# Optimization experiments

Measured on AMD Instinct MI355X. Metric: run time of the kernel, lower is better.

Reference implementation:

```python
import jax, jax.numpy as jnp
import numpy as np

HID = 128; H = 8; D = HID // H; L = 2; IN = 128; OUT = 32
ND = 20000; NF = 50000; E = 400000
SQRT_D = float(np.sqrt(D))
LN_EPS = 1e-5


def setup_inputs() -> dict:
    key = jax.random.key(0)
    ks = jax.random.split(key, 16)
    s = 1.0 / np.sqrt(HID)
    n = lambda k, sh, sc=1.0: jax.random.normal(k, sh, jnp.float32) * sc
    return dict(
        x_device=n(ks[0], (ND, IN)),
        x_feature=n(ks[1], (NF, IN)),
        e_df_src=jax.random.randint(ks[2], (E,), 0, ND),
        e_df_dst=jax.random.randint(ks[3], (E,), 0, NF),
        e_fd_src=jax.random.randint(ks[4], (E,), 0, NF),
        e_fd_dst=jax.random.randint(ks[5], (E,), 0, ND),
        W_dev_in=n(ks[6], (IN, HID), s), b_dev_in=jnp.zeros((HID,), jnp.float32),
        W_feat_in=n(ks[7], (IN, HID), s), b_feat_in=jnp.zeros((HID,), jnp.float32),
        Wk=n(ks[8], (L, 2, HID, HID), s), bk=jnp.zeros((L, 2, HID), jnp.float32),
        Wq=n(ks[9], (L, 2, HID, HID), s), bq=jnp.zeros((L, 2, HID), jnp.float32),
        Wv=n(ks[10], (L, 2, HID, HID), s), bv=jnp.zeros((L, 2, HID), jnp.float32),
        a_rel=n(ks[11], (L, 2, H, D, D), 1.0 / np.sqrt(D)),
        m_rel=n(ks[12], (L, 2, H, D, D), 1.0 / np.sqrt(D)),
        p_rel=jnp.ones((L, 2, H), jnp.float32),
        Wa=n(ks[13], (L, 2, HID, HID), s), ba=jnp.zeros((L, 2, HID), jnp.float32),
        skip=jnp.ones((L, 2), jnp.float32),
        ln_g=jnp.ones((L, 2, HID), jnp.float32), ln_b=jnp.zeros((L, 2, HID), jnp.float32),
        W_out=n(ks[14], (HID, OUT), s), b_out=jnp.zeros((OUT,), jnp.float32),
    )


def _layer_norm(x, g, b):
    m = x.mean(-1, keepdims=True)
    v = ((x - m) ** 2).mean(-1, keepdims=True)
    return (x - m) * jax.lax.rsqrt(v + LN_EPS) * g + b


def _edge_agg(q_dst, k_src, v_src, a_r, m_r, p_r, src, dst, n_dst):
    # per-edge-type relation transforms of source k/v: [N_src,H,D]
    kt = jnp.einsum('nhd,hde->nhe', k_src, a_r)
    vt = jnp.einsum('nhd,hde->nhe', v_src, m_r)
    # per-edge attention logits [E,H], scaled by relation prior
    logit = (q_dst[dst] * kt[src]).sum(-1) * p_r / SQRT_D
    # segment softmax over incoming edges of each dst node (per edge type)
    mx = jax.ops.segment_max(logit, dst, num_segments=n_dst)
    ex = jnp.exp(logit - mx[dst])
    sm = jax.ops.segment_sum(ex, dst, num_segments=n_dst)
    alpha = ex / (sm[dst] + 1e-16)
    # attention-weighted message scatter-sum -> [n_dst,H,D]
    return jax.ops.segment_sum(vt[src] * alpha[..., None], dst, num_segments=n_dst)


def _forward(x_device, x_feature, W_dev_in, b_dev_in, W_feat_in, b_feat_in,
             Wk, bk, Wq, bq, Wv, bv, a_rel, m_rel, p_rel, Wa, ba, skip,
             ln_g, ln_b, W_out, b_out, e_df_src, e_df_dst, e_fd_src, e_fd_dst):
    x_d = jax.nn.relu(x_device @ W_dev_in + b_dev_in)
    x_f = jax.nn.relu(x_feature @ W_feat_in + b_feat_in)
    for l in range(L):
        xs = (x_d, x_f)  # node-type 0 = device, 1 = feature
        k = [(xs[t] @ Wk[l, t] + bk[l, t]).reshape(-1, H, D) for t in range(2)]
        q = [(xs[t] @ Wq[l, t] + bq[l, t]).reshape(-1, H, D) for t in range(2)]
        v = [(xs[t] @ Wv[l, t] + bv[l, t]).reshape(-1, H, D) for t in range(2)]
        # edge type 0: device -> feature ; edge type 1: feature -> device
        agg_f = _edge_agg(q[1], k[0], v[0], a_rel[l, 0], m_rel[l, 0], p_rel[l, 0],
                          e_df_src, e_df_dst, NF)
        agg_d = _edge_agg(q[0], k[1], v[1], a_rel[l, 1], m_rel[l, 1], p_rel[l, 1],
                          e_fd_src, e_fd_dst, ND)
        new = []
        for t, agg in ((0, agg_d), (1, agg_f)):
            o = jax.nn.gelu(agg.reshape(-1, HID), approximate=False) @ Wa[l, t] + ba[l, t]
            sk = jax.nn.sigmoid(skip[l, t])
            o = sk * o + (1.0 - sk) * xs[t]              # HGTConv skip
            new.append(_layer_norm(xs[t] + o, ln_g[l, t], ln_b[l, t]))  # wrapper residual+LN (dropout=identity in eval)
        x_d, x_f = new
    return x_d @ W_out + b_out


def reference(x_device, x_feature, e_df_src, e_df_dst, e_fd_src, e_fd_dst,
              W_dev_in, b_dev_in, W_feat_in, b_feat_in, Wk, bk, Wq, bq, Wv, bv,
              a_rel, m_rel, p_rel, Wa, ba, skip, ln_g, ln_b, W_out, b_out):
    return _forward(x_device, x_feature, W_dev_in, b_dev_in, W_feat_in, b_feat_in,
                    Wk, bk, Wq, bq, Wv, bv, a_rel, m_rel, p_rel, Wa, ba, skip,
                    ln_g, ln_b, W_out, b_out, e_df_src, e_df_dst, e_fd_src, e_fd_dst)
```

## Files before the change

### kernel.cpp

```cpp
#include <hip/hip_runtime.h>
#include <math.h>

#define ND 20000
#define NF 50000
#define NE 400000
#define NT (NF + ND)
#define NBKT 256
#define BKTW 274

typedef __attribute__((ext_vector_type(8))) short short8;
typedef __attribute__((ext_vector_type(4))) float f32x4;
typedef unsigned short us;

static __device__ __forceinline__ us f2bf(float f) {
    unsigned u = __builtin_bit_cast(unsigned, f);
    u += 0x7FFF + ((u >> 16) & 1);
    return (us)(u >> 16);
}
static __device__ __forceinline__ float bf2f(us h) {
    return __builtin_bit_cast(float, (unsigned)h << 16);
}
static __device__ __forceinline__ float bflo(unsigned u) {
    return __builtin_bit_cast(float, u << 16);
}
static __device__ __forceinline__ float bfhi(unsigned u) {
    return __builtin_bit_cast(float, u & 0xFFFF0000u);
}
static __device__ __forceinline__ float gelu_f(float x) {
    return 0.5f * x * (1.0f + erff(x * 0.70710678118654752f));
}

__global__ void k_hist_prep(const int* __restrict__ dA, const int* __restrict__ dB,
                            int* __restrict__ blockhist, int HB,
                            const float* __restrict__ W_dev_in, const float* __restrict__ W_feat_in,
                            const float* __restrict__ Wq, const float* __restrict__ Wk,
                            const float* __restrict__ Wv, const float* __restrict__ Wa,
                            const float* __restrict__ b_dev_in, const float* __restrict__ b_feat_in,
                            const float* __restrict__ bq, const float* __restrict__ bk,
                            const float* __restrict__ bv, const float* __restrict__ ba,
                            const float* __restrict__ a_rel, const float* __restrict__ m_rel,
                            const float* __restrict__ p_rel,
                            us* __restrict__ WT, float* __restrict__ B_all) {
    __shared__ int hist[NBKT];
    if ((int)blockIdx.x < HB) {
        hist[threadIdx.x] = 0;
        __syncthreads();
        int base_e = blockIdx.x * 4096;
        #pragma unroll
        for (int j = 0; j < 16; ++j) {
            int e = base_e + j * 256 + threadIdx.x;
            if (e < 2 * NE) {
                int g = (e < NE) ? dA[e] : (NF + dB[e - NE]);
                atomicAdd(&hist[g / BKTW], 1);
            }
        }
        __syncthreads();
        blockhist[blockIdx.x * NBKT + threadIdx.x] = hist[threadIdx.x];
        return;
    }
    int idx = (blockIdx.x - HB) * 256 + threadIdx.x;
    if (idx < 18 * 16384) {
        int k = idx & 127, c = (idx >> 7) & 127, id = idx >> 14;
        float val;
        if (id == 0) val = W_dev_in[k * 128 + c];
        else if (id == 1) val = W_feat_in[k * 128 + c];
        else if (id < 6) val = Wq[(id - 2) * 16384 + k * 128 + c];
        else if (id < 10) {
            int lt = id - 6, h = c >> 4, e = c & 15;
            const float* A = a_rel + (lt * 8 + h) * 256;
            const float* Ws = Wk + lt * 16384 + k * 128 + h * 16;
            float sm = 0.f;
            #pragma unroll
            for (int d = 0; d < 16; ++d) sm += Ws[d] * A[d * 16 + e];
            val = sm * p_rel[lt * 8 + h] * 0.25f;
        } else if (id < 14) {
            int lt = id - 10, h = c >> 4, e = c & 15;
            const float* A = m_rel + (lt * 8 + h) * 256;
            const float* Ws = Wv + lt * 16384 + k * 128 + h * 16;
            float sm = 0.f;
            #pragma unroll
            for (int d = 0; d < 16; ++d) sm += Ws[d] * A[d * 16 + e];
            val = sm;
        } else val = Wa[(id - 14) * 16384 + k * 128 + c];
        WT[(size_t)id * 16384 + (((c * 128 + k)) ^ ((c & 7) << 3))] = f2bf(val);
    } else {
        int j = idx - 18 * 16384;
        if (j >= 18 * 128) return;
        int c = j & 127, id = j >> 7;
        float v;
        if (id == 0) v = b_dev_in[c];
        else if (id == 1) v = b_feat_in[c];
        else if (id < 6) v = bq[(id - 2) * 128 + c];
        else if (id < 10) {
            int lt = id - 6, h = c >> 4, e = c & 15;
            const float* A = a_rel + (lt * 8 + h) * 256;
            const float* bs = bk + lt * 128 + h * 16;
            float sm = 0.f;
            #pragma unroll
            for (int d = 0; d < 16; ++d) sm += bs[d] * A[d * 16 + e];
            v = sm * p_rel[lt * 8 + h] * 0.25f;
        } else if (id < 14) {
            int lt = id - 10, h = c >> 4, e = c & 15;
            const float* A = m_rel + (lt * 8 + h) * 256;
            const float* bs = bv + lt * 128 + h * 16;
            float sm = 0.f;
            #pragma unroll
            for (int d = 0; d < 16; ++d) sm += bs[d] * A[d * 16 + e];
            v = sm;
        } else v = ba[(id - 14) * 128 + c];
        B_all[j] = v;
    }
}

__global__ void k_scanA(int* __restrict__ blockhist, int* __restrict__ totals, int HB) {
    __shared__ int sd[256];
    int b = blockIdx.x, t = threadIdx.x;
    int v = (t < HB) ? blockhist[t * NBKT + b] : 0;
    sd[t] = v; __syncthreads();
    for (int off = 1; off < 256; off <<= 1) {
        int add = (t >= off) ? sd[t - off] : 0;
        __syncthreads();
        sd[t] += add;
        __syncthreads();
    }
    if (t < HB) blockhist[t * NBKT + b] = sd[t] - v;
    if (t == 255) totals[b] = sd[255];
}

__global__ void k_scanB(const int* __restrict__ totals, int* __restrict__ base) {
    __shared__ int sd[256];
    int t = threadIdx.x;
    int v = totals[t];
    sd[t] = v; __syncthreads();
    for (int off = 1; off < 256; off <<= 1) {
        int add = (t >= off) ? sd[t - off] : 0;
        __syncthreads();
        sd[t] += add;
        __syncthreads();
    }
    base[t] = sd[t] - v;
    if (t == 255) base[256] = sd[255];
}

__global__ void k_scatter(const int* __restrict__ sA, const int* __restrict__ dA,
                          const int* __restrict__ sB, const int* __restrict__ dB,
                          const int* __restrict__ blockhist, const int* __restrict__ base,
                          uint2* __restrict__ pairs) {
    __shared__ int lcur[NBKT];
    int t = threadIdx.x;
    lcur[t] = base[t] + blockhist[blockIdx.x * NBKT + t];
    __syncthreads();
    int base_e = blockIdx.x * 4096;
    #pragma unroll
    for (int j = 0; j < 16; ++j) {
        int e = base_e + j * 256 + t;
        if (e < 2 * NE) {
            int src, g;
            if (e < NE) { src = sA[e]; g = dA[e]; }
            else        { src = sB[e - NE]; g = NF + dB[e - NE]; }
            int pos = atomicAdd(&lcur[g / BKTW], 1);
            pairs[pos] = make_uint2((unsigned)src, (unsigned)g);
        }
    }
}

__global__ void k_bucket_csr(const uint2* __restrict__ pairs, const int* __restrict__ base,
                             int* __restrict__ rs, int* __restrict__ esrc) {
    __shared__ int cnt[BKTW];
    __shared__ int excl[BKTW];
    int b = blockIdx.x, t = threadIdx.x;
    int start = base[b], end = base[b + 1];
    int g0 = b * BKTW;
    for (int i = t; i < BKTW; i += 256) cnt[i] = 0;
    __syncthreads();
    for (int i = start + t; i < end; i += 256)
        atomicAdd(&cnt[(int)pairs[i].y - g0], 1);
    __syncthreads();
    if (t < 64) {
        int lane = t;
        int vals[5]; int s = 0;
        #pragma unroll
        for (int j = 0; j < 5; ++j) {
            int i = lane * 5 + j;
            vals[j] = (i < BKTW) ? cnt[i] : 0;
            s += vals[j];
        }
        int incl = s;
        #pragma unroll
        for (int off = 1; off < 64; off <<= 1) {
            int n = __shfl_up(incl, off);
            if (lane >= off) incl += n;
        }
        int run = incl - s;
        #pragma unroll
        for (int j = 0; j < 5; ++j) {
            int i = lane * 5 + j;
            if (i < BKTW) excl[i] = run;
            run += vals[j];
        }
    }
    __syncthreads();
    int nloc = min(BKTW, NT - g0);
    for (int i = t; i < nloc; i += 256) rs[g0 + i] = start + excl[i];
    if (b == NBKT - 1 && t == 0) rs[NT] = base[NBKT];
    __syncthreads();
    for (int i = start + t; i < end; i += 256) {
        uint2 p = pairs[i];
        int pos = start + atomicAdd(&excl[(int)p.y - g0], 1);
        esrc[pos] = (int)p.x;
    }
}

template<int MODE, int AF32, int RELU>
__global__ __launch_bounds__(256) void mfma_gemm2(
    const void* __restrict__ X0, const void* __restrict__ X1,
    const us* __restrict__ WT0, const float* __restrict__ Ball,
    us* __restrict__ Y0, us* __restrict__ Y1,
    int N0, int N1, int GB0, int widbase,
    us* __restrict__ K0, us* __restrict__ K1,
    const float* __restrict__ skipv, const float* __restrict__ lng,
    const float* __restrict__ lnb) {
    __shared__ us Wlds[16384];
    const int type = (blockIdx.x >= (unsigned)GB0) ? 1 : 0;
    const int bx = blockIdx.x - (type ? GB0 : 0);
    const int N = type ? N1 : N0;
    const void* Xv = type ? X1 : X0;
    const int NP = (MODE == 1) ? 3 : 1;

    const int lane = threadIdx.x & 63;
    const int wave = threadIdx.x >> 6;
    const int row_base = bx * 128 + wave * 32;
    const int l15 = lane & 15, lg = lane >> 4;
    const int kbase = lg * 8;

    const char* gsrc0 = (const char*)(WT0 + (size_t)(widbase + type) * 16384)
                        + wave * 8192 + lane * 16;
    {
        char* ldst = (char*)Wlds + wave * 8192;
        #pragma unroll
        for (int i = 0; i < 8; ++i) {
            __builtin_amdgcn_global_load_lds(
                (const __attribute__((address_space(1))) void*)(gsrc0 + i * 1024),
                (__attribute__((address_space(3))) void*)(ldst + i * 1024),
                16, 0, 0);
        }
    }

    short8 a[2][4];
    #pragma unroll
    for (int mf = 0; mf < 2; ++mf) {
        int r = row_base + mf * 16 + l15;
        r = r < N ? r : N - 1;
        if (AF32) {
            const float* Xf = (const float*)Xv + (size_t)r * 128;
            #pragma unroll
            for (int kf = 0; kf < 4; ++kf) {
                float4 lo = *(const float4*)(Xf + kf * 32 + kbase);
                float4 hi = *(const float4*)(Xf + kf * 32 + kbase + 4);
                short8 t;
                t[0] = (short)f2bf(lo.x); t[1] = (short)f2bf(lo.y);
                t[2] = (short)f2bf(lo.z); t[3] = (short)f2bf(lo.w);
                t[4] = (short)f2bf(hi.x); t[5] = (short)f2bf(hi.y);
                t[6] = (short)f2bf(hi.z); t[7] = (short)f2bf(hi.w);
                a[mf][kf] = t;
            }
        } else {
            const us* Xb = (const us*)Xv + (size_t)r * 128;
            #pragma unroll
            for (int kf = 0; kf < 4; ++kf)
                a[mf][kf] = *(const short8*)(Xb + kf * 32 + kbase);
        }
    }

    __syncthreads();

    const unsigned swz = (unsigned)((l15 & 7) << 4);

    for (int p = 0; p < NP; ++p) {
        const int wid = widbase + type + 4 * p;
        const float* bias = Ball + wid * 128;

        f32x4 acc[2][8];
        #pragma unroll
        for (int mf = 0; mf < 2; ++mf)
            #pragma unroll
            for (int cf = 0; cf < 8; ++cf) acc[mf][cf] = (f32x4){0.f, 0.f, 0.f, 0.f};

        #pragma unroll
        for (int cf = 0; cf < 8; ++cf) {
            const unsigned rowbyte = (unsigned)((cf * 16 + l15) * 256 + kbase * 2);
            #pragma unroll
            for (int kf = 0; kf < 4; ++kf) {
                short8 b = *(const short8*)((const char*)Wlds + ((rowbyte + kf * 64) ^ swz));
                acc[0][cf] = __builtin_amdgcn_mfma_f32_16x16x32_bf16(a[0][kf], b, acc[0][cf], 0, 0, 0);
                acc[1][cf] = __builtin_amdgcn_mfma_f32_16x16x32_bf16(a[1][kf], b, acc[1][cf], 0, 0, 0);
            }
        }

        if (MODE == 1 && p + 1 < NP) {
            __syncthreads();
            const char* gsrc = (const char*)(WT0 + (size_t)(widbase + type + 4 * (p + 1)) * 16384)
                               + wave * 8192 + lane * 16;
            char* ldst = (char*)Wlds + wave * 8192;
            #pragma unroll
            for (int i = 0; i < 8; ++i) {
                __builtin_amdgcn_global_load_lds(
                    (const __attribute__((address_space(1))) void*)(gsrc + i * 1024),
                    (__attribute__((address_space(3))) void*)(ldst + i * 1024),
                    16, 0, 0);
            }
        }

        float bval[8];
        #pragma unroll
        for (int cf = 0; cf < 8; ++cf) bval[cf] = bias[cf * 16 + l15];

        if (MODE == 2) {
            const int lt = widbase - 14 + type;
            float sk = 1.f / (1.f + __expf(-skipv[lt]));
            float gv[8], bv2[8];
            #pragma unroll
            for (int cf = 0; cf < 8; ++cf) {
                gv[cf]  = lng[(size_t)lt * 128 + cf * 16 + l15];
                bv2[cf] = lnb[(size_t)lt * 128 + cf * 16 + l15];
            }
            us* xw = type ? K1 : K0;
            #pragma unroll
            for (int mf = 0; mf < 2; ++mf)
                #pragma unroll
                for (int r = 0; r < 4; ++r) {
                    int grow = row_base + mf * 16 + lg * 4 + r;
                    if (grow >= N) continue;
                    float t[8];
                    float sum = 0.f;
                    #pragma unroll
                    for (int cf = 0; cf < 8; ++cf) {
                        float o = acc[mf][cf][r] + bval[cf];
                        float x = bf2f(xw[(size_t)grow * 128 + cf * 16 + l15]);
                        t[cf] = (2.f - sk) * x + sk * o;
                        sum += t[cf];
                    }
                    sum += __shfl_xor(sum, 1); sum += __shfl_xor(sum, 2);
                    sum += __shfl_xor(sum, 4); sum += __shfl_xor(sum, 8);
                    float mean = sum * (1.0f / 128.0f);
                    float vs = 0.f;
                    #pragma unroll
                    for (int cf = 0; cf < 8; ++cf) { t[cf] -= mean; vs += t[cf] * t[cf]; }
                    vs += __shfl_xor(vs, 1); vs += __shfl_xor(vs, 2);
                    vs += __shfl_xor(vs, 4); vs += __shfl_xor(vs, 8);
                    float inv = rsqrtf(vs * (1.0f / 128.0f) + 1e-5f);
                    #pragma unroll
                    for (int cf = 0; cf < 8; ++cf)
                        xw[(size_t)grow * 128 + cf * 16 + l15] = f2bf(t[cf] * inv * gv[cf] + bv2[cf]);
                }
        } else {
            #pragma unroll
            for (int mf = 0; mf < 2; ++mf)
                #pragma unroll
                for (int r = 0; r < 4; ++r) {
                    int grow = row_base + mf * 16 + lg * 4 + r;
                    if (grow >= N) continue;
                    #pragma unroll
                    for (int cf = 0; cf < 8; ++cf) {
                        float v = acc[mf][cf][r] + bval[cf];
                        if (RELU) v = fmaxf(v, 0.f);
                        us val = f2bf(v);
                        int col = cf * 16 + l15;
                        if (MODE == 0 || p == 0) {
                            (type ? Y1 : Y0)[(size_t)grow * 128 + col] = val;
                        } else {
                            (type ? K1 : K0)[(size_t)grow * 256 + (p - 1) * 128 + col] = val;
                        }
                    }
                }
        }

        if (MODE == 1 && p + 1 < NP) __syncthreads();
    }
}

__global__ __launch_bounds__(256) void gemm_out_k(
    const us* __restrict__ X, const float* __restrict__ W,
    const float* __restrict__ bias, float* __restrict__ Y, int N) {
    __shared__ float Ws[128 * 32];
    __shared__ float Xs[8][128];
    const int tid = threadIdx.x;
    const int row0 = blockIdx.x * 8;
    #pragma unroll
    for (int it = 0; it < 16; ++it) Ws[it * 256 + tid] = W[it * 256 + tid];
    #pragma unroll
    for (int it = 0; it < 2; ++it) {
        int idx = it * 256 + tid;
        int rr = idx >> 6, kp = idx & 63;
        int gr = row0 + rr;
        unsigned u = (gr < N) ? *(const unsigned*)(X + (size_t)gr * 128 + kp * 2) : 0u;
        Xs[rr][kp * 2]     = bflo(u);
        Xs[rr][kp * 2 + 1] = bfhi(u);
    }
    __syncthreads();
    const int rr = tid >> 5, c = tid & 31;
    float acc = bias[c];
    #pragma unroll 8
    for (int k = 0; k < 128; ++k)
        acc = fmaf(Xs[rr][k], Ws[k * 32 + c], acc);
    int gr = row0 + rr;
    if (gr < N) Y[(size_t)gr * 32 + c] = acc;
}

#define EDGE_STEP(kc, vc, pidx)                                        \
    {                                                                  \
        float part = qv[0] * bflo(kc.x);                               \
        part = fmaf(qv[1], bfhi(kc.x), part);                          \
        part = fmaf(qv[2], bflo(kc.y), part);                          \
        part = fmaf(qv[3], bfhi(kc.y), part);                          \
        part = fmaf(qv[4], bflo(kc.z), part);                          \
        part = fmaf(qv[5], bfhi(kc.z), part);                          \
        part = fmaf(qv[6], bflo(kc.w), part);                          \
        part = fmaf(qv[7], bfhi(kc.w), part);                          \
        part += __shfl_xor(part, 1);                                   \
        float w = ((pidx) < p1) ? __expf(part) : 0.f;                  \
        s += w;                                                        \
        a[0] = fmaf(w, bflo(vc.x), a[0]);                              \
        a[1] = fmaf(w, bfhi(vc.x), a[1]);                              \
        a[2] = fmaf(w, bflo(vc.y), a[2]);                              \
        a[3] = fmaf(w, bfhi(vc.y), a[3]);                              \
        a[4] = fmaf(w, bflo(vc.z), a[4]);                              \
        a[5] = fmaf(w, bfhi(vc.z), a[5]);                              \
        a[6] = fmaf(w, bflo(vc.w), a[6]);                              \
        a[7] = fmaf(w, bfhi(vc.w), a[7]);                              \
    }

__global__ __launch_bounds__(256) void edge_agg5(
    const us* __restrict__ qf, const us* __restrict__ qd,
    const us* __restrict__ kvf, const us* __restrict__ kvd,
    const int* __restrict__ rs, const int* __restrict__ esrc,
    us* __restrict__ aggf, us* __restrict__ aggd) {
    int g = (blockIdx.x * 256 + threadIdx.x) >> 4;
    int li = threadIdx.x & 15;
    if (g >= NT) return;
    const us *q, *kv; us* agg; int dst;
    if (g < NF) { dst = g;      q = qf; kv = kvd; agg = aggf; }
    else        { dst = g - NF; q = qd; kv = kvf; agg = aggd; }

    uint4 qb = *(const uint4*)(q + (size_t)dst * 128 + li * 8);
    float qv[8];
    qv[0] = bflo(qb.x); qv[1] = bfhi(qb.x);
    qv[2] = bflo(qb.y); qv[3] = bfhi(qb.y);
    qv[4] = bflo(qb.z); qv[5] = bfhi(qb.z);
    qv[6] = bflo(qb.w); qv[7] = bfhi(qb.w);

    const int p0 = rs[g], p1 = rs[g + 1];
    float s = 0.f;
    float a[8];
    #pragma unroll
    for (int j = 0; j < 8; ++j) a[j] = 0.f;

    const size_t loff = (size_t)li * 8;
    uint4 kA0, vA0, kA1, vA1, kB0, vB0, kB1, vB1;
    int sN0, sN1, sN2, sN3;

    if (p0 < p1) {
        const int last = p1 - 1;
        int i0 = p0, i1 = min(p0 + 1, last), i2 = min(p0 + 2, last), i3 = min(p0 + 3, last);
        int s0 = esrc[i0], s1 = esrc[i1], s2 = esrc[i2], s3 = esrc[i3];
        kA0 = *(const uint4*)(kv + (size_t)s0 * 256 + loff);
        vA0 = *(const uint4*)(kv + (size_t)s0 * 256 + 128 + loff);
        kA1 = *(const uint4*)(kv + (size_t)s1 * 256 + loff);
        vA1 = *(const uint4*)(kv + (size_t)s1 * 256 + 128 + loff);
        kB0 = *(const uint4*)(kv + (size_t)s2 * 256 + loff);
        vB0 = *(const uint4*)(kv + (size_t)s2 * 256 + 128 + loff);
        kB1 = *(const uint4*)(kv + (size_t)s3 * 256 + loff);
        vB1 = *(const uint4*)(kv + (size_t)s3 * 256 + 128 + loff);
        sN0 = esrc[min(p0 + 4, last)];
        sN1 = esrc[min(p0 + 5, last)];
        sN2 = esrc[min(p0 + 6, last)];
        sN3 = esrc[min(p0 + 7, last)];

        for (int p = p0; p < p1; p += 4) {
            const int lastc = last;
            EDGE_STEP(kA0, vA0, p);
            EDGE_STEP(kA1, vA1, p + 1);
            kA0 = *(const uint4*)(kv + (size_t)sN0 * 256 + loff);
            vA0 = *(const uint4*)(kv + (size_t)sN0 * 256 + 128 + loff);
            kA1 = *(const uint4*)(kv + (size_t)sN1 * 256 + loff);
            vA1 = *(const uint4*)(kv + (size_t)sN1 * 256 + 128 + loff);
            sN0 = esrc[min(p + 8, lastc)];
            sN1 = esrc[min(p + 9, lastc)];
            EDGE_STEP(kB0, vB0, p + 2);
            EDGE_STEP(kB1, vB1, p + 3);
            kB0 = *(const uint4*)(kv + (size_t)sN2 * 256 + loff);
            vB0 = *(const uint4*)(kv + (size_t)sN2 * 256 + 128 + loff);
            kB1 = *(const uint4*)(kv + (size_t)sN3 * 256 + loff);
            vB1 = *(const uint4*)(kv + (size_t)sN3 * 256 + 128 + loff);
            sN2 = esrc[min(p + 10, lastc)];
            sN3 = esrc[min(p + 11, lastc)];
        }
    }

    float r = 1.0f / (s + 1e-16f);
    unsigned o[4];
    #pragma unroll
    for (int j = 0; j < 4; ++j) {
        us lo = f2bf(gelu_f(a[2 * j] * r));
        us hi = f2bf(gelu_f(a[2 * j + 1] * r));
        o[j] = (unsigned)lo | ((unsigned)hi << 16);
    }
    *(uint4*)(agg + (size_t)dst * 128 + li * 8) = make_uint4(o[0], o[1], o[2], o[3]);
}

extern "C" void kernel_launch(void* const* d_in, const int* in_sizes, int n_in,
                              void* d_out, int out_size, void* d_ws, size_t ws_size,
                              hipStream_t stream) {
    const float* x_device = (const float*)d_in[0];
    const float* x_feature = (const float*)d_in[1];
    const int* e_df_src = (const int*)d_in[2];
    const int* e_df_dst = (const int*)d_in[3];
    const int* e_fd_src = (const int*)d_in[4];
    const int* e_fd_dst = (const int*)d_in[5];
    const float* W_dev_in = (const float*)d_in[6];
    const float* b_dev_in = (const float*)d_in[7];
    const float* W_feat_in = (const float*)d_in[8];
    const float* b_feat_in = (const float*)d_in[9];
    const float* Wk = (const float*)d_in[10];
    const float* bk = (const float*)d_in[11];
    const float* Wq = (const float*)d_in[12];
    const float* bq = (const float*)d_in[13];
    const float* Wv = (const float*)d_in[14];
    const float* bv = (const float*)d_in[15];
    const float* a_rel = (const float*)d_in[16];
    const float* m_rel = (const float*)d_in[17];
    const float* p_rel = (const float*)d_in[18];
    const float* Wa = (const float*)d_in[19];
    const float* ba = (const float*)d_in[20];
    const float* skip = (const float*)d_in[21];
    const float* ln_g = (const float*)d_in[22];
    const float* ln_b = (const float*)d_in[23];
    const float* W_out = (const float*)d_in[24];
    const float* b_out = (const float*)d_in[25];

    char* ws = (char*)d_ws;
    size_t off = 0;
    auto alloc = [&](size_t bytes) -> void* {
        void* p = ws + off;
        off = (off + bytes + 255) & ~(size_t)255;
        return p;
    };
    us* xd     = (us*)alloc((size_t)ND * 128 * 2);
    us* xf     = (us*)alloc((size_t)NF * 128 * 2);
    us* q_d    = (us*)alloc((size_t)ND * 128 * 2);
    us* q_f    = (us*)alloc((size_t)NF * 128 * 2);
    us* kv_d   = (us*)alloc((size_t)ND * 256 * 2);
    us* kv_f   = (us*)alloc((size_t)NF * 256 * 2);
    us* agg_d  = (us*)alloc((size_t)ND * 128 * 2);
    us* agg_f  = (us*)alloc((size_t)NF * 128 * 2);
    us* WT     = (us*)alloc((size_t)18 * 16384 * 2);
    float* B_all = (float*)alloc(18 * 128 * 4);
    int* rs     = (int*)alloc((size_t)(NT + 1) * 4);
    int* esrc   = (int*)alloc((size_t)(2 * NE + 8) * 4);
    uint2* pairs = (uint2*)alloc((size_t)2 * NE * 8);
    int* blockhist = (int*)alloc((size_t)200 * NBKT * 4);
    int* totals = (int*)alloc(NBKT * 4);
    int* base   = (int*)alloc((NBKT + 1) * 4);

    const int HB = (2 * NE + 4095) / 4096;
    const int PB = (18 * 16384 + 18 * 128 + 255) / 256;

    k_hist_prep<<<HB + PB, 256, 0, stream>>>(
        e_df_dst, e_fd_dst, blockhist, HB,
        W_dev_in, W_feat_in, Wq, Wk, Wv, Wa,
        b_dev_in, b_feat_in, bq, bk, bv, ba,
        a_rel, m_rel, p_rel, WT, B_all);
    k_scanA<<<NBKT, 256, 0, stream>>>(blockhist, totals, HB);
    k_scanB<<<1, 256, 0, stream>>>(totals, base);
    k_scatter<<<HB, 256, 0, stream>>>(e_df_src, e_df_dst, e_fd_src, e_fd_dst,
                                      blockhist, base, pairs);
    k_bucket_csr<<<NBKT, 256, 0, stream>>>(pairs, base, rs, esrc);

    const int GBD = (ND + 127) / 128, GBF = (NF + 127) / 128;

    mfma_gemm2<0, 1, 1><<<GBD + GBF, 256, 0, stream>>>(
        x_device, x_feature, WT, B_all, xd, xf, ND, NF, GBD, 0,
        nullptr, nullptr, nullptr, nullptr, nullptr);

    for (int l = 0; l < 2; ++l) {
        mfma_gemm2<1, 0, 0><<<GBD + GBF, 256, 0, stream>>>(
            xd, xf, WT, B_all, q_d, q_f, ND, NF, GBD, 2 + l * 2,
            kv_d, kv_f, nullptr, nullptr, nullptr);

        edge_agg5<<<((NT * 16) + 255) / 256, 256, 0, stream>>>(
            q_f, q_d, kv_f, kv_d, rs, esrc, agg_f, agg_d);

        mfma_gemm2<2, 0, 0><<<GBD + GBF, 256, 0, stream>>>(
            agg_d, agg_f, WT, B_all, nullptr, nullptr, ND, NF, GBD, 14 + l * 2,
            xd, xf, skip, ln_g, ln_b);
    }

    gemm_out_k<<<(ND + 7) / 8, 256, 0, stream>>>(xd, W_out, b_out, (float*)d_out, ND);
}
```

Before: 267.7 us.

## Fuse edge aggregation with output GEMM and LayerNorm; fold scanB into consumers

```diff
diff --git a/kernel.cpp b/kernel.cpp
--- a/kernel.cpp
+++ b/kernel.cpp
@@ -127,28 +127,22 @@
     if (t == 255) totals[b] = sd[255];
 }
 
-__global__ void k_scanB(const int* __restrict__ totals, int* __restrict__ base) {
-    __shared__ int sd[256];
-    int t = threadIdx.x;
-    int v = totals[t];
-    sd[t] = v; __syncthreads();
-    for (int off = 1; off < 256; off <<= 1) {
-        int add = (t >= off) ? sd[t - off] : 0;
-        __syncthreads();
-        sd[t] += add;
-        __syncthreads();
-    }
-    base[t] = sd[t] - v;
-    if (t == 255) base[256] = sd[255];
-}
-
 __global__ void k_scatter(const int* __restrict__ sA, const int* __restrict__ dA,
                           const int* __restrict__ sB, const int* __restrict__ dB,
-                          const int* __restrict__ blockhist, const int* __restrict__ base,
+                          const int* __restrict__ blockhist, const int* __restrict__ totals,
                           uint2* __restrict__ pairs) {
     __shared__ int lcur[NBKT];
+    __shared__ int sdb[NBKT];
     int t = threadIdx.x;
-    lcur[t] = base[t] + blockhist[blockIdx.x * NBKT + t];
+    int tv = totals[t];
+    sdb[t] = tv; __syncthreads();
+    for (int off = 1; off < 256; off <<= 1) {
+        int add = (t >= off) ? sdb[t - off] : 0;
+        __syncthreads();
+        sdb[t] += add;
+        __syncthreads();
+    }
+    lcur[t] = (sdb[t] - tv) + blockhist[blockIdx.x * NBKT + t];
     __syncthreads();
     int base_e = blockIdx.x * 4096;
     #pragma unroll
@@ -164,12 +158,24 @@
     }
 }
 
-__global__ void k_bucket_csr(const uint2* __restrict__ pairs, const int* __restrict__ base,
+__global__ void k_bucket_csr(const uint2* __restrict__ pairs, const int* __restrict__ totals,
                              int* __restrict__ rs, int* __restrict__ esrc) {
     __shared__ int cnt[BKTW];
     __shared__ int excl[BKTW];
+    __shared__ int sdb[NBKT];
+    __shared__ int sde[NBKT];
     int b = blockIdx.x, t = threadIdx.x;
-    int start = base[b], end = base[b + 1];
+    int tv = totals[t];
+    sdb[t] = tv; __syncthreads();
+    for (int off = 1; off < 256; off <<= 1) {
+        int add = (t >= off) ? sdb[t - off] : 0;
+        __syncthreads();
+        sdb[t] += add;
+        __syncthreads();
+    }
+    sde[t] = sdb[t] - tv;
+    __syncthreads();
+    int start = sde[b], end = sdb[b];
     int g0 = b * BKTW;
     for (int i = t; i < BKTW; i += 256) cnt[i] = 0;
     __syncthreads();
@@ -202,7 +208,7 @@
     __syncthreads();
     int nloc = min(BKTW, NT - g0);
     for (int i = t; i < nloc; i += 256) rs[g0 + i] = start + excl[i];
-    if (b == NBKT - 1 && t == 0) rs[NT] = base[NBKT];
+    if (b == NBKT - 1 && t == 0) rs[NT] = sdb[255];
     __syncthreads();
     for (int i = start + t; i < end; i += 256) {
         uint2 p = pairs[i];
@@ -217,9 +223,7 @@
     const us* __restrict__ WT0, const float* __restrict__ Ball,
     us* __restrict__ Y0, us* __restrict__ Y1,
     int N0, int N1, int GB0, int widbase,
-    us* __restrict__ K0, us* __restrict__ K1,
-    const float* __restrict__ skipv, const float* __restrict__ lng,
-    const float* __restrict__ lnb) {
+    us* __restrict__ K0, us* __restrict__ K1) {
     __shared__ us Wlds[16384];
     const int type = (blockIdx.x >= (unsigned)GB0) ? 1 : 0;
     const int bx = blockIdx.x - (type ? GB0 : 0);
@@ -233,14 +237,14 @@
     const int l15 = lane & 15, lg = lane >> 4;
     const int kbase = lg * 8;
 
-    const char* gsrc0 = (const char*)(WT0 + (size_t)(widbase + type) * 16384)
-                        + wave * 8192 + lane * 16;
     {
+        const char* gsrc = (const char*)(WT0 + (size_t)(widbase + type) * 16384)
+                           + wave * 8192 + lane * 16;
         char* ldst = (char*)Wlds + wave * 8192;
         #pragma unroll
         for (int i = 0; i < 8; ++i) {
             __builtin_amdgcn_global_load_lds(
-                (const __attribute__((address_space(1))) void*)(gsrc0 + i * 1024),
+                (const __attribute__((address_space(1))) void*)(gsrc + i * 1024),
                 (__attribute__((address_space(3))) void*)(ldst + i * 1024),
                 16, 0, 0);
         }
@@ -315,65 +319,25 @@
         #pragma unroll
         for (int cf = 0; cf < 8; ++cf) bval[cf] = bias[cf * 16 + l15];
 
-        if (MODE == 2) {
-            const int lt = widbase - 14 + type;
-            float sk = 1.f / (1.f + __expf(-skipv[lt]));
-            float gv[8], bv2[8];
-            #pragma unroll
-            for (int cf = 0; cf < 8; ++cf) {
-                gv[cf]  = lng[(size_t)lt * 128 + cf * 16 + l15];
-                bv2[cf] = lnb[(size_t)lt * 128 + cf * 16 + l15];
-            }
-            us* xw = type ? K1 : K0;
-            #pragma unroll
-            for (int mf = 0; mf < 2; ++mf)
+        #pragma unroll
+        for (int mf = 0; mf < 2; ++mf)
+            #pragma unroll
+            for (int r = 0; r < 4; ++r) {
+                int grow = row_base + mf * 16 + lg * 4 + r;
+                if (grow >= N) continue;
                 #pragma unroll
-                for (int r = 0; r < 4; ++r) {
-                    int grow = row_base + mf * 16 + lg * 4 + r;
-                    if (grow >= N) continue;
-                    float t[8];
-                    float sum = 0.f;
-                    #pragma unroll
-                    for (int cf = 0; cf < 8; ++cf) {
-                        float o = acc[mf][cf][r] + bval[cf];
-                        float x = bf2f(xw[(size_t)grow * 128 + cf * 16 + l15]);
-                        t[cf] = (2.f - sk) * x + sk * o;
-                        sum += t[cf];
-                    }
-                    sum += __shfl_xor(sum, 1); sum += __shfl_xor(sum, 2);
-                    sum += __shfl_xor(sum, 4); sum += __shfl_xor(sum, 8);
-                    float mean = sum * (1.0f / 128.0f);
-                    float vs = 0.f;
-                    #pragma unroll
-                    for (int cf = 0; cf < 8; ++cf) { t[cf] -= mean; vs += t[cf] * t[cf]; }
-                    vs += __shfl_xor(vs, 1); vs += __shfl_xor(vs, 2);
-                    vs += __shfl_xor(vs, 4); vs += __shfl_xor(vs, 8);
-                    float inv = rsqrtf(vs * (1.0f / 128.0f) + 1e-5f);
-                    #pragma unroll
-                    for (int cf = 0; cf < 8; ++cf)
-                        xw[(size_t)grow * 128 + cf * 16 + l15] = f2bf(t[cf] * inv * gv[cf] + bv2[cf]);
-                }
-        } else {
-            #pragma unroll
-            for (int mf = 0; mf < 2; ++mf)
-                #pragma unroll
-                for (int r = 0; r < 4; ++r) {
-                    int grow = row_base + mf * 16 + lg * 4 + r;
-                    if (grow >= N) continue;
-                    #pragma unroll
-                    for (int cf = 0; cf < 8; ++cf) {
-                        float v = acc[mf][cf][r] + bval[cf];
-                        if (RELU) v = fmaxf(v, 0.f);
-                        us val = f2bf(v);
-                        int col = cf * 16 + l15;
-                        if (MODE == 0 || p == 0) {
-                            (type ? Y1 : Y0)[(size_t)grow * 128 + col] = val;
-                        } else {
-                            (type ? K1 : K0)[(size_t)grow * 256 + (p - 1) * 128 + col] = val;
-                        }
+                for (int cf = 0; cf < 8; ++cf) {
+                    float v = acc[mf][cf][r] + bval[cf];
+                    if (RELU) v = fmaxf(v, 0.f);
+                    us val = f2bf(v);
+                    int col = cf * 16 + l15;
+                    if (MODE == 0 || p == 0) {
+                        (type ? Y1 : Y0)[(size_t)grow * 128 + col] = val;
+                    } else {
+                        (type ? K1 : K0)[(size_t)grow * 256 + (p - 1) * 128 + col] = val;
                     }
                 }
-        }
+            }
 
         if (MODE == 1 && p + 1 < NP) __syncthreads();
     }
@@ -430,82 +394,179 @@
         a[7] = fmaf(w, bfhi(vc.w), a[7]);                              \
     }
 
-__global__ __launch_bounds__(256) void edge_agg5(
-    const us* __restrict__ qf, const us* __restrict__ qd,
-    const us* __restrict__ kvf, const us* __restrict__ kvd,
+__global__ __launch_bounds__(256) void edge_fused(
+    const us* __restrict__ q_d, const us* __restrict__ q_f,
+    const us* __restrict__ kv_d, const us* __restrict__ kv_f,
     const int* __restrict__ rs, const int* __restrict__ esrc,
-    us* __restrict__ aggf, us* __restrict__ aggd) {
-    int g = (blockIdx.x * 256 + threadIdx.x) >> 4;
-    int li = threadIdx.x & 15;
-    if (g >= NT) return;
-    const us *q, *kv; us* agg; int dst;
-    if (g < NF) { dst = g;      q = qf; kv = kvd; agg = aggf; }
-    else        { dst = g - NF; q = qd; kv = kvf; agg = aggd; }
-
-    uint4 qb = *(const uint4*)(q + (size_t)dst * 128 + li * 8);
-    float qv[8];
-    qv[0] = bflo(qb.x); qv[1] = bfhi(qb.x);
-    qv[2] = bflo(qb.y); qv[3] = bfhi(qb.y);
-    qv[4] = bflo(qb.z); qv[5] = bfhi(qb.z);
-    qv[6] = bflo(qb.w); qv[7] = bfhi(qb.w);
-
-    const int p0 = rs[g], p1 = rs[g + 1];
-    float s = 0.f;
-    float a[8];
-    #pragma unroll
-    for (int j = 0; j < 8; ++j) a[j] = 0.f;
-
-    const size_t loff = (size_t)li * 8;
-    uint4 kA0, vA0, kA1, vA1, kB0, vB0, kB1, vB1;
-    int sN0, sN1, sN2, sN3;
-
-    if (p0 < p1) {
-        const int last = p1 - 1;
-        int i0 = p0, i1 = min(p0 + 1, last), i2 = min(p0 + 2, last), i3 = min(p0 + 3, last);
-        int s0 = esrc[i0], s1 = esrc[i1], s2 = esrc[i2], s3 = esrc[i3];
-        kA0 = *(const uint4*)(kv + (size_t)s0 * 256 + loff);
-        vA0 = *(const uint4*)(kv + (size_t)s0 * 256 + 128 + loff);
-        kA1 = *(const uint4*)(kv + (size_t)s1 * 256 + loff);
-        vA1 = *(const uint4*)(kv + (size_t)s1 * 256 + 128 + loff);
-        kB0 = *(const uint4*)(kv + (size_t)s2 * 256 + loff);
-        vB0 = *(const uint4*)(kv + (size_t)s2 * 256 + 128 + loff);
-        kB1 = *(const uint4*)(kv + (size_t)s3 * 256 + loff);
-        vB1 = *(const uint4*)(kv + (size_t)s3 * 256 + 128 + loff);
-        sN0 = esrc[min(p0 + 4, last)];
-        sN1 = esrc[min(p0 + 5, last)];
-        sN2 = esrc[min(p0 + 6, last)];
-        sN3 = esrc[min(p0 + 7, last)];
-
-        for (int p = p0; p < p1; p += 4) {
-            const int lastc = last;
-            EDGE_STEP(kA0, vA0, p);
-            EDGE_STEP(kA1, vA1, p + 1);
-            kA0 = *(const uint4*)(kv + (size_t)sN0 * 256 + loff);
-            vA0 = *(const uint4*)(kv + (size_t)sN0 * 256 + 128 + loff);
-            kA1 = *(const uint4*)(kv + (size_t)sN1 * 256 + loff);
-            vA1 = *(const uint4*)(kv + (size_t)sN1 * 256 + 128 + loff);
-            sN0 = esrc[min(p + 8, lastc)];
-            sN1 = esrc[min(p + 9, lastc)];
-            EDGE_STEP(kB0, vB0, p + 2);
-            EDGE_STEP(kB1, vB1, p + 3);
-            kB0 = *(const uint4*)(kv + (size_t)sN2 * 256 + loff);
-            vB0 = *(const uint4*)(kv + (size_t)sN2 * 256 + 128 + loff);
-            kB1 = *(const uint4*)(kv + (size_t)sN3 * 256 + loff);
-            vB1 = *(const uint4*)(kv + (size_t)sN3 * 256 + 128 + loff);
-            sN2 = esrc[min(p + 10, lastc)];
-            sN3 = esrc[min(p + 11, lastc)];
-        }
-    }
-
-    float r = 1.0f / (s + 1e-16f);
-    unsigned o[4];
-    #pragma unroll
-    for (int j = 0; j < 4; ++j) {
-        us lo = f2bf(gelu_f(a[2 * j] * r));
-        us hi = f2bf(gelu_f(a[2 * j + 1] * r));
-        o[j] = (unsigned)lo | ((unsigned)hi << 16);
-    }
-    *(uint4*)(agg + (size_t)dst * 128 + li * 8) = make_uint4(o[0], o[1], o[2], o[3]);
+    const us* __restrict__ WT0, const float* __restrict__ Ball, int widbase,
+    us* __restrict__ xd, us* __restrict__ xf,
+    const float* __restrict__ skipv, const float* __restrict__ lng,
+    const float* __restrict__ lnb, int GB0) {
+    __shared__ us Wlds[16384];
+    __shared__ us Alds[8192];
+    const int type = (blockIdx.x >= (unsigned)GB0) ? 1 : 0;
+    const int bx = blockIdx.x - (type ? GB0 : 0);
+    const int N = type ? NF : ND;
+    const us* q  = type ? q_f : q_d;
+    const us* kv = type ? kv_d : kv_f;
+    us* xw = type ? xf : xd;
+    const int goff = type ? 0 : NF;
+    const int row0 = bx * 64;
+    const int wid = widbase + type;
+
+    const int t = threadIdx.x;
+    const int lane = t & 63;
+    const int wave = t >> 6;
+    const int l15 = lane & 15, lg = lane >> 4;
+    const int kbase = lg * 8;
+    const int li = t & 15;
+
+    {
+        const char* gsrc = (const char*)(WT0 + (size_t)wid * 16384) + wave * 8192 + lane * 16;
+        char* ldst = (char*)Wlds + wave * 8192;
+        #pragma unroll
+        for (int i = 0; i < 8; ++i) {
+            __builtin_amdgcn_global_load_lds(
+                (const __attribute__((address_space(1))) void*)(gsrc + i * 1024),
+                (__attribute__((address_space(3))) void*)(ldst + i * 1024),
+                16, 0, 0);
+        }
+    }
+
+    for (int it = 0; it < 4; ++it) {
+        int dst_local = it * 16 + (t >> 4);
+        int dst = row0 + dst_local;
+        unsigned o0 = 0, o1 = 0, o2 = 0, o3 = 0;
+        if (dst < N) {
+            int g = dst + goff;
+            uint4 qb = *(const uint4*)(q + (size_t)dst * 128 + li * 8);
+            float qv[8];
+            qv[0] = bflo(qb.x); qv[1] = bfhi(qb.x);
+            qv[2] = bflo(qb.y); qv[3] = bfhi(qb.y);
+            qv[4] = bflo(qb.z); qv[5] = bfhi(qb.z);
+            qv[6] = bflo(qb.w); qv[7] = bfhi(qb.w);
+
+            const int p0 = rs[g], p1 = rs[g + 1];
+            float s = 0.f;
+            float a[8];
+            #pragma unroll
+            for (int j = 0; j < 8; ++j) a[j] = 0.f;
+
+            const size_t loff = (size_t)li * 8;
+            if (p0 < p1) {
+                const int last = p1 - 1;
+                uint4 kA0, vA0, kA1, vA1, kB0, vB0, kB1, vB1;
+                int sN0, sN1, sN2, sN3;
+                int s0 = esrc[p0], s1 = esrc[min(p0 + 1, last)];
+                int s2 = esrc[min(p0 + 2, last)], s3 = esrc[min(p0 + 3, last)];
+                kA0 = *(const uint4*)(kv + (size_t)s0 * 256 + loff);
+                vA0 = *(const uint4*)(kv + (size_t)s0 * 256 + 128 + loff);
+                kA1 = *(const uint4*)(kv + (size_t)s1 * 256 + loff);
+                vA1 = *(const uint4*)(kv + (size_t)s1 * 256 + 128 + loff);
+                kB0 = *(const uint4*)(kv + (size_t)s2 * 256 + loff);
+                vB0 = *(const uint4*)(kv + (size_t)s2 * 256 + 128 + loff);
+                kB1 = *(const uint4*)(kv + (size_t)s3 * 256 + loff);
+                vB1 = *(const uint4*)(kv + (size_t)s3 * 256 + 128 + loff);
+                sN0 = esrc[min(p0 + 4, last)];
+                sN1 = esrc[min(p0 + 5, last)];
+                sN2 = esrc[min(p0 + 6, last)];
+                sN3 = esrc[min(p0 + 7, last)];
+
+                for (int p = p0; p < p1; p += 4) {
+                    EDGE_STEP(kA0, vA0, p);
+                    EDGE_STEP(kA1, vA1, p + 1);
+                    kA0 = *(const uint4*)(kv + (size_t)sN0 * 256 + loff);
+                    vA0 = *(const uint4*)(kv + (size_t)sN0 * 256 + 128 + loff);
+                    kA1 = *(const uint4*)(kv + (size_t)sN1 * 256 + loff);
+                    vA1 = *(const uint4*)(kv + (size_t)sN1 * 256 + 128 + loff);
+                    sN0 = esrc[min(p + 8, last)];
+                    sN1 = esrc[min(p + 9, last)];
+                    EDGE_STEP(kB0, vB0, p + 2);
+                    EDGE_STEP(kB1, vB1, p + 3);
+                    kB0 = *(const uint4*)(kv + (size_t)sN2 * 256 + loff);
+                    vB0 = *(const uint4*)(kv + (size_t)sN2 * 256 + 128 + loff);
+                    kB1 = *(const uint4*)(kv + (size_t)sN3 * 256 + loff);
+                    vB1 = *(const uint4*)(kv + (size_t)sN3 * 256 + 128 + loff);
+                    sN2 = esrc[min(p + 10, last)];
+                    sN3 = esrc[min(p + 11, last)];
+                }
+            }
+            float r = 1.0f / (s + 1e-16f);
+            us lo, hi;
+            lo = f2bf(gelu_f(a[0] * r)); hi = f2bf(gelu_f(a[1] * r));
+            o0 = (unsigned)lo | ((unsigned)hi << 16);
+            lo = f2bf(gelu_f(a[2] * r)); hi = f2bf(gelu_f(a[3] * r));
+            o1 = (unsigned)lo | ((unsigned)hi << 16);
+            lo = f2bf(gelu_f(a[4] * r)); hi = f2bf(gelu_f(a[5] * r));
+            o2 = (unsigned)lo | ((unsigned)hi << 16);
+            lo = f2bf(gelu_f(a[6] * r)); hi = f2bf(gelu_f(a[7] * r));
+            o3 = (unsigned)lo | ((unsigned)hi << 16);
+        }
+        unsigned byteoff = ((unsigned)(dst_local * 256 + li * 16)) ^ ((unsigned)(dst_local & 7) << 4);
+        *(uint4*)((char*)Alds + byteoff) = make_uint4(o0, o1, o2, o3);
+    }
+
+    __syncthreads();
+
+    short8 av[4];
+    {
+        int row_local = wave * 16 + l15;
+        unsigned rb = (unsigned)(row_local * 256);
+        unsigned sx = (unsigned)((row_local & 7) << 4);
+        #pragma unroll
+        for (int kf = 0; kf < 4; ++kf)
+            av[kf] = *(const short8*)((const char*)Alds + ((rb + kf * 64 + lg * 16) ^ sx));
+    }
+
+    const unsigned swz = (unsigned)((l15 & 7) << 4);
+    f32x4 acc[8];
+    #pragma unroll
+    for (int cf = 0; cf < 8; ++cf) acc[cf] = (f32x4){0.f, 0.f, 0.f, 0.f};
+    #pragma unroll
+    for (int cf = 0; cf < 8; ++cf) {
+        const unsigned rowbyte = (unsigned)((cf * 16 + l15) * 256 + kbase * 2);
+        #pragma unroll
+        for (int kf = 0; kf < 4; ++kf) {
+            short8 b = *(const short8*)((const char*)Wlds + ((rowbyte + kf * 64) ^ swz));
+            acc[cf] = __builtin_amdgcn_mfma_f32_16x16x32_bf16(av[kf], b, acc[cf], 0, 0, 0);
+        }
+    }
+
+    const int lt = widbase - 14 + type;
+    float sk = 1.f / (1.f + __expf(-skipv[lt]));
+    float bval[8], gv[8], bv2[8];
+    #pragma unroll
+    for (int cf = 0; cf < 8; ++cf) {
+        bval[cf] = Ball[wid * 128 + cf * 16 + l15];
+        gv[cf]   = lng[(size_t)lt * 128 + cf * 16 + l15];
+        bv2[cf]  = lnb[(size_t)lt * 128 + cf * 16 + l15];
+    }
+    #pragma unroll
+    for (int r = 0; r < 4; ++r) {
+        int grow = row0 + wave * 16 + lg * 4 + r;
+        if (grow >= N) continue;
+        float tt[8];
+        float sum = 0.f;
+        #pragma unroll
+        for (int cf = 0; cf < 8; ++cf) {
+            float o = acc[cf][r] + bval[cf];
+            float x = bf2f(xw[(size_t)grow * 128 + cf * 16 + l15]);
+            tt[cf] = (2.f - sk) * x + sk * o;
+            sum += tt[cf];
+        }
+        sum += __shfl_xor(sum, 1); sum += __shfl_xor(sum, 2);
+        sum += __shfl_xor(sum, 4); sum += __shfl_xor(sum, 8);
+        float mean = sum * (1.0f / 128.0f);
+        float vs = 0.f;
+        #pragma unroll
+        for (int cf = 0; cf < 8; ++cf) { tt[cf] -= mean; vs += tt[cf] * tt[cf]; }
+        vs += __shfl_xor(vs, 1); vs += __shfl_xor(vs, 2);
+        vs += __shfl_xor(vs, 4); vs += __shfl_xor(vs, 8);
+        float inv = rsqrtf(vs * (1.0f / 128.0f) + 1e-5f);
+        #pragma unroll
+        for (int cf = 0; cf < 8; ++cf)
+            xw[(size_t)grow * 128 + cf * 16 + l15] = f2bf(tt[cf] * inv * gv[cf] + bv2[cf]);
+    }
 }
 
 extern "C" void kernel_launch(void* const* d_in, const int* in_sizes, int n_in,
@@ -551,8 +612,6 @@
     us* q_f    = (us*)alloc((size_t)NF * 128 * 2);
     us* kv_d   = (us*)alloc((size_t)ND * 256 * 2);
     us* kv_f   = (us*)alloc((size_t)NF * 256 * 2);
-    us* agg_d  = (us*)alloc((size_t)ND * 128 * 2);
-    us* agg_f  = (us*)alloc((size_t)NF * 128 * 2);
     us* WT     = (us*)alloc((size_t)18 * 16384 * 2);
     float* B_all = (float*)alloc(18 * 128 * 4);
     int* rs     = (int*)alloc((size_t)(NT + 1) * 4);
@@ -560,7 +619,6 @@
     uint2* pairs = (uint2*)alloc((size_t)2 * NE * 8);
     int* blockhist = (int*)alloc((size_t)200 * NBKT * 4);
     int* totals = (int*)alloc(NBKT * 4);
-    int* base   = (int*)alloc((NBKT + 1) * 4);
 
     const int HB = (2 * NE + 4095) / 4096;
     const int PB = (18 * 16384 + 18 * 128 + 255) / 256;
@@ -571,28 +629,25 @@
         b_dev_in, b_feat_in, bq, bk, bv, ba,
         a_rel, m_rel, p_rel, WT, B_all);
     k_scanA<<<NBKT, 256, 0, stream>>>(blockhist, totals, HB);
-    k_scanB<<<1, 256, 0, stream>>>(totals, base);
     k_scatter<<<HB, 256, 0, stream>>>(e_df_src, e_df_dst, e_fd_src, e_fd_dst,
-                                      blockhist, base, pairs);
-    k_bucket_csr<<<NBKT, 256, 0, stream>>>(pairs, base, rs, esrc);
+                                      blockhist, totals, pairs);
+    k_bucket_csr<<<NBKT, 256, 0, stream>>>(pairs, totals, rs, esrc);
 
     const int GBD = (ND + 127) / 128, GBF = (NF + 127) / 128;
+    const int GBD64 = (ND + 63) / 64, GBF64 = (NF + 63) / 64;
 
     mfma_gemm2<0, 1, 1><<<GBD + GBF, 256, 0, stream>>>(
         x_device, x_feature, WT, B_all, xd, xf, ND, NF, GBD, 0,
-        nullptr, nullptr, nullptr, nullptr, nullptr);
+        nullptr, nullptr);
 
     for (int l = 0; l < 2; ++l) {
         mfma_gemm2<1, 0, 0><<<GBD + GBF, 256, 0, stream>>>(
             xd, xf, WT, B_all, q_d, q_f, ND, NF, GBD, 2 + l * 2,
-            kv_d, kv_f, nullptr, nullptr, nullptr);
-
-        edge_agg5<<<((NT * 16) + 255) / 256, 256, 0, stream>>>(
-            q_f, q_d, kv_f, kv_d, rs, esrc, agg_f, agg_d);
-
-        mfma_gemm2<2, 0, 0><<<GBD + GBF, 256, 0, stream>>>(
-            agg_d, agg_f, WT, B_all, nullptr, nullptr, ND, NF, GBD, 14 + l * 2,
-            xd, xf, skip, ln_g, ln_b);
+            kv_d, kv_f);
+
+        edge_fused<<<GBD64 + GBF64, 256, 0, stream>>>(
+            q_d, q_f, kv_d, kv_f, rs, esrc, WT, B_all, 14 + l * 2,
+            xd, xf, skip, ln_g, ln_b, GBD64);
     }
 
     gemm_out_k<<<(ND + 7) / 8, 256, 0, stream>>>(xd, W_out, b_out, (float*)d_out, ND);
```

Result: no change. 263.5 us (-1.6%).
